# Optimization experiments

Measured on AMD Instinct MI355X. Metric: run time of the kernel, lower is better.

## Reference

```python
import jax, jax.numpy as jnp
import numpy as np

N_HEAD = 16
N_KV = 4
ROT = 128  # rotary_dim == head_dim
BASE = 10000
N_CTX = 1024


def make_sincos(n_ctx, rotary_dim, base):
    # GPT-NeoX style (rotary_adjacent_pairs=False): freq repeated twice
    pos = jnp.arange(n_ctx, dtype=jnp.float32)
    dim = jnp.arange(rotary_dim // 2, dtype=jnp.float32)
    freq = jnp.float32(base) ** (dim / (rotary_dim / 2))
    freq = jnp.tile(freq, 2)  # [rotary_dim]
    angles = pos[:, None] / freq[None, :]  # [n_ctx, rotary_dim]
    return jnp.sin(angles), jnp.cos(angles)


def setup_inputs() -> dict:
    key = jax.random.key(0)
    ks = jax.random.split(key, 5)
    B, T, C = 8, 1024, 2048
    r = N_HEAD // N_KV
    Ckv = C // r
    s = 0.02
    x = jax.random.normal(ks[0], (B, T, C), jnp.float32)
    wq = jax.random.normal(ks[1], (C, C), jnp.float32) * s
    wk = jax.random.normal(ks[2], (C, Ckv), jnp.float32) * s
    wv = jax.random.normal(ks[3], (C, Ckv), jnp.float32) * s
    wo = jax.random.normal(ks[4], (C, C), jnp.float32) * s
    sin, cos = make_sincos(N_CTX, ROT, BASE)
    return dict(x=x, wq=wq, wk=wk, wv=wv, wo=wo, sin=sin, cos=cos)


def _rope(x, sin, cos):
    # x: [B, H, T, hd]; rotary applied to first ROT dims (here ROT == hd)
    T = x.shape[2]
    n = ROT // 2
    x_rot = x[..., :ROT]
    x_pass = x[..., ROT:]
    # rotate_every_two (NeoX style): [x0..x_{n-1}, x_n..] -> [-x_n.., x0..]
    x_flip = jnp.concatenate([-x_rot[..., n:], x_rot[..., :n]], axis=-1)
    c = cos[None, None, :T, :]
    s = sin[None, None, :T, :]
    x_rotated = x_rot * c + x_flip * s
    return jnp.concatenate([x_rotated, x_pass], axis=-1)


def reference(x, wq, wk, wv, wo, sin, cos):
    B, T, C = x.shape
    H = N_HEAD
    hd = C // H
    r = H // N_KV
    q = (x @ wq).reshape(B, T, H, hd).transpose(0, 2, 1, 3)  # [B,H,T,hd]
    # Original: repeat_interleave along seq dim then view(B,T,H,hd).
    # Equivalent to tiling the kv channel vector r times per position.
    k = jnp.tile(x @ wk, (1, 1, r)).reshape(B, T, H, hd).transpose(0, 2, 1, 3)
    v = jnp.tile(x @ wv, (1, 1, r)).reshape(B, T, H, hd).transpose(0, 2, 1, 3)
    q = _rope(q, sin, cos)
    k = _rope(k, sin, cos)
    att = jnp.einsum('bhqd,bhkd->bhqk', q, k) / jnp.sqrt(jnp.float32(hd))
    causal = jnp.tril(jnp.ones((T, T), dtype=bool))
    att = jnp.where(causal[None, None], att, -jnp.inf)
    att = jax.nn.softmax(att, axis=-1)
    y = jnp.einsum('bhqk,bhkd->bhqd', att, v)
    y = y.transpose(0, 2, 1, 3).reshape(B, T, C)
    return y @ wo
```

## Files before the change

kernel.cpp:

```cpp
#include <hip/hip_runtime.h>

typedef __attribute__((ext_vector_type(8))) short short8;
typedef __attribute__((ext_vector_type(4))) float f32x4;

#define B_    8
#define T_    1024
#define C_    2048
#define H_    16
#define HKV_  4
#define HD_   128
#define M_    8192
#define NQKV_ 3072
#define KDIM_ 2048

__device__ __forceinline__ unsigned short f2bf(float f) {
  unsigned u = __float_as_uint(f);
  u += 0x7FFF + ((u >> 16) & 1);
  return (unsigned short)(u >> 16);
}
__device__ __forceinline__ float bf2f(unsigned short h) {
  return __uint_as_float(((unsigned)h) << 16);
}

__device__ __forceinline__ void async16(const unsigned short* g, unsigned short* l) {
  __builtin_amdgcn_global_load_lds(
      (const unsigned int __attribute__((address_space(1)))*)g,
      (unsigned int __attribute__((address_space(3)))*)l,
      16, 0, 0);
}

__global__ __launch_bounds__(256) void cvt_bf16_kernel(const float* __restrict__ in,
                                                       unsigned short* __restrict__ out) {
  int idx = blockIdx.x * 256 + threadIdx.x;
  float4 v = ((const float4*)in)[idx];
  ushort4 o;
  o.x = f2bf(v.x); o.y = f2bf(v.y); o.z = f2bf(v.z); o.w = f2bf(v.w);
  ((ushort4*)out)[idx] = o;
}

__global__ __launch_bounds__(256) void tpose_f32_bf16(const float* __restrict__ in,
                                                      unsigned short* __restrict__ out,
                                                      int Cc, int ldo) {
  __shared__ unsigned short tile[32][33];
  int c0 = blockIdx.x * 32, r0 = blockIdx.y * 32;
  int tx = threadIdx.x, ty = threadIdx.y;
#pragma unroll
  for (int j = 0; j < 4; j++)
    tile[ty + j * 8][tx] = f2bf(in[(size_t)(r0 + ty + j * 8) * Cc + c0 + tx]);
  __syncthreads();
#pragma unroll
  for (int j = 0; j < 4; j++)
    out[(size_t)(c0 + ty + j * 8) * ldo + r0 + tx] = tile[tx][ty + j * 8];
}

__global__ __launch_bounds__(256) void vtpose(const unsigned short* __restrict__ qkv,
                                              unsigned short* __restrict__ vt) {
  __shared__ unsigned short tile[32][33];
  int b = blockIdx.z;
  int c0 = blockIdx.x * 32, t0 = blockIdx.y * 32;
  int tx = threadIdx.x, ty = threadIdx.y;
  const unsigned short* src = qkv + (size_t)b * T_ * NQKV_ + 2560;
#pragma unroll
  for (int j = 0; j < 4; j++)
    tile[ty + j * 8][tx] = src[(size_t)(t0 + ty + j * 8) * NQKV_ + c0 + tx];
  __syncthreads();
  unsigned short* dst = vt + (size_t)b * 512 * T_;
#pragma unroll
  for (int j = 0; j < 4; j++)
    dst[(size_t)(c0 + ty + j * 8) * T_ + t0 + tx] = tile[tx][ty + j * 8];
}

__global__ __launch_bounds__(256) void rope_kernel(const unsigned short* __restrict__ qkv,
                                                   const float* __restrict__ sinp,
                                                   const float* __restrict__ cosp,
                                                   unsigned short* __restrict__ qatt,
                                                   unsigned short* __restrict__ katt) {
  int m = blockIdx.x;
  int b = m >> 10, t = m & 1023;
  int tid = threadIdx.x;
  int d = tid & 63;
  const unsigned short* row = qkv + (size_t)m * NQKV_;
  float c0 = cosp[t * 128 + d], s0 = sinp[t * 128 + d];
  float c1 = cosp[t * 128 + d + 64], s1 = sinp[t * 128 + d + 64];
#pragma unroll
  for (int h0 = 0; h0 < 16; h0 += 4) {
    int h = h0 + (tid >> 6);
    float x0 = bf2f(row[h * 128 + d]);
    float x1 = bf2f(row[h * 128 + d + 64]);
    size_t o = ((size_t)(b * 16 + h) * 1024 + t) * 128 + d;
    qatt[o]      = f2bf(x0 * c0 - x1 * s0);
    qatt[o + 64] = f2bf(x1 * c1 + x0 * s1);
  }
  {
    int kh = tid >> 6;
    float x0 = bf2f(row[2048 + kh * 128 + d]);
    float x1 = bf2f(row[2048 + kh * 128 + d + 64]);
    size_t o = ((size_t)(b * 4 + kh) * 1024 + t) * 128 + d;
    katt[o]      = f2bf(x0 * c0 - x1 * s0);
    katt[o + 64] = f2bf(x1 * c1 + x0 * s1);
  }
}

template <int OUTF32>
__global__ __launch_bounds__(256) void gemm_bf16(const unsigned short* __restrict__ A,
                                                 const unsigned short* __restrict__ BT,
                                                 void* __restrict__ Cout, int N) {
  __shared__ unsigned short lA[128 * 32];
  __shared__ unsigned short lB[128 * 32];
  const int K = KDIM_;
  int tid = threadIdx.x;
  int lane = tid & 63;
  int w = tid >> 6;
  int quad = lane >> 4, l16 = lane & 15;
  int bm = blockIdx.y, bn = blockIdx.x;
  const unsigned short* Ab = A + (size_t)bm * 128 * K;
  const unsigned short* Bb = BT + (size_t)bn * 128 * K;
  int i0 = tid, i1 = tid + 256;
  int ra0 = i0 >> 2, ca0 = (i0 & 3) * 8;
  int ra1 = i1 >> 2, ca1 = (i1 & 3) * 8;
  int wm = (w >> 1) * 64, wn = (w & 1) * 64;
  f32x4 acc[4][4] = {};
  for (int k0 = 0; k0 < K; k0 += 32) {
    __syncthreads();
    async16(Ab + (size_t)ra0 * K + k0 + ca0, &lA[i0 * 8]);
    async16(Ab + (size_t)ra1 * K + k0 + ca1, &lA[i1 * 8]);
    async16(Bb + (size_t)ra0 * K + k0 + ca0, &lB[i0 * 8]);
    async16(Bb + (size_t)ra1 * K + k0 + ca1, &lB[i1 * 8]);
    __syncthreads();
    short8 af[4], bfr[4];
#pragma unroll
    for (int mt = 0; mt < 4; mt++)
      af[mt] = *(const short8*)&lA[(wm + mt * 16 + l16) * 32 + quad * 8];
#pragma unroll
    for (int nt = 0; nt < 4; nt++)
      bfr[nt] = *(const short8*)&lB[(wn + nt * 16 + l16) * 32 + quad * 8];
#pragma unroll
    for (int mt = 0; mt < 4; mt++)
#pragma unroll
      for (int nt = 0; nt < 4; nt++)
        acc[mt][nt] = __builtin_amdgcn_mfma_f32_16x16x32_bf16(af[mt], bfr[nt], acc[mt][nt], 0, 0, 0);
  }
#pragma unroll
  for (int mt = 0; mt < 4; mt++) {
#pragma unroll
    for (int nt = 0; nt < 4; nt++) {
      int n = bn * 128 + wn + nt * 16 + l16;
#pragma unroll
      for (int r = 0; r < 4; r++) {
        int m = bm * 128 + wm + mt * 16 + quad * 4 + r;
        if (OUTF32)
          ((float*)Cout)[(size_t)m * N + n] = acc[mt][nt][r];
        else
          ((unsigned short*)Cout)[(size_t)m * N + n] = f2bf(acc[mt][nt][r]);
      }
    }
  }
}

__global__ __launch_bounds__(256, 4) void attn_kernel(const unsigned short* __restrict__ Q,
                                                      const unsigned short* __restrict__ Km,
                                                      const unsigned short* __restrict__ Vt,
                                                      unsigned short* __restrict__ Y) {
  __shared__ __align__(16) unsigned short lK[8192];
  __shared__ __align__(16) unsigned short lV[8192];
  int tid = threadIdx.x;
  int lane = tid & 63, w = tid >> 6;
  int quad = lane >> 4, l16 = lane & 15;
  int qt = 15 - blockIdx.x;
  int bh = blockIdx.y;
  int b = bh >> 4, h = bh & 15, kh = h & 3;
  int qrow0 = qt * 64 + w * 16;
  const unsigned short* Qb = Q + ((size_t)bh * T_ + qrow0) * 128;
  const unsigned short* Kb = Km + (size_t)(b * 4 + kh) * T_ * 128;
  const unsigned short* Vb = Vt + (size_t)(b * 4 + kh) * 128 * T_;
  short8 qf[4];
#pragma unroll
  for (int ks = 0; ks < 4; ks++)
    qf[ks] = *(const short8*)&Qb[l16 * 128 + ks * 32 + quad * 8];
  f32x4 o[8] = {};
  float m_r[4] = {-1e30f, -1e30f, -1e30f, -1e30f};
  float l_r[4] = {0.f, 0.f, 0.f, 0.f};
  const float sc = 0.12751744690989f;
  unsigned short* pb = &lK[w * 1152];
  int ntile = qt + 1;
  for (int kt = 0; kt < ntile; kt++) {
    int n0 = kt * 64;
    __syncthreads();
#pragma unroll
    for (int j = 0; j < 4; j++) {
      int i = tid + j * 256;
      async16(Kb + (size_t)(n0 + ((i >> 2) & 63)) * 128 + (i >> 8) * 32 + (i & 3) * 8,
              &lK[i * 8]);
    }
#pragma unroll
    for (int j = 0; j < 4; j++) {
      int i = tid + j * 256;
      async16(Vb + (size_t)((i >> 2) & 127) * T_ + n0 + (i >> 9) * 32 + (i & 3) * 8,
              &lV[i * 8]);
    }
    __syncthreads();
    f32x4 s[4] = {};
#pragma unroll
    for (int ct = 0; ct < 4; ct++) {
#pragma unroll
      for (int ks = 0; ks < 4; ks++) {
        short8 kf = *(const short8*)&lK[ks * 2048 + (ct * 16 + l16) * 32 + quad * 8];
        s[ct] = __builtin_amdgcn_mfma_f32_16x16x32_bf16(qf[ks], kf, s[ct], 0, 0, 0);
      }
    }
#pragma unroll
    for (int ct = 0; ct < 4; ct++)
#pragma unroll
      for (int r = 0; r < 4; r++)
        s[ct][r] *= sc;
    if (kt == qt) {
#pragma unroll
      for (int ct = 0; ct < 4; ct++) {
        int n = n0 + ct * 16 + l16;
#pragma unroll
        for (int r = 0; r < 4; r++) {
          int q = qrow0 + quad * 4 + r;
          if (n > q) s[ct][r] = -1e30f;
        }
      }
    }
    float mn[4], alpha[4];
#pragma unroll
    for (int r = 0; r < 4; r++) {
      float v = fmaxf(fmaxf(s[0][r], s[1][r]), fmaxf(s[2][r], s[3][r]));
#pragma unroll
      for (int off = 1; off < 16; off <<= 1)
        v = fmaxf(v, __shfl_xor(v, off));
      mn[r] = fmaxf(m_r[r], v);
      alpha[r] = exp2f(m_r[r] - mn[r]);
      m_r[r] = mn[r];
    }
#pragma unroll
    for (int ct = 0; ct < 4; ct++)
#pragma unroll
      for (int r = 0; r < 4; r++)
        s[ct][r] = exp2f(s[ct][r] - mn[r]);
#pragma unroll
    for (int r = 0; r < 4; r++) {
      float v = s[0][r] + s[1][r] + s[2][r] + s[3][r];
#pragma unroll
      for (int off = 1; off < 16; off <<= 1)
        v += __shfl_xor(v, off);
      l_r[r] = l_r[r] * alpha[r] + v;
    }
#pragma unroll
    for (int dt = 0; dt < 8; dt++)
#pragma unroll
      for (int r = 0; r < 4; r++)
        o[dt][r] *= alpha[r];
    __syncthreads();
#pragma unroll
    for (int ct = 0; ct < 4; ct++)
#pragma unroll
      for (int r = 0; r < 4; r++)
        pb[(quad * 4 + r) * 72 + ct * 16 + l16] = f2bf(s[ct][r]);
    __builtin_amdgcn_s_waitcnt(0xC07F);
#pragma unroll
    for (int ks2 = 0; ks2 < 2; ks2++) {
      short8 pa = *(const short8*)&pb[l16 * 72 + ks2 * 32 + quad * 8];
#pragma unroll
      for (int dt = 0; dt < 8; dt++) {
        short8 vf = *(const short8*)&lV[ks2 * 4096 + (dt * 16 + l16) * 32 + quad * 8];
        o[dt] = __builtin_amdgcn_mfma_f32_16x16x32_bf16(pa, vf, o[dt], 0, 0, 0);
      }
    }
  }
#pragma unroll
  for (int r = 0; r < 4; r++) {
    int q = qrow0 + quad * 4 + r;
    float inv = 1.f / l_r[r];
    size_t base = ((size_t)(b * 1024 + q)) * 2048 + h * 128 + l16;
#pragma unroll
    for (int dt = 0; dt < 8; dt++)
      Y[base + dt * 16] = f2bf(o[dt][r] * inv);
  }
}

extern "C" void kernel_launch(void* const* d_in, const int* in_sizes, int n_in,
                              void* d_out, int out_size, void* d_ws, size_t ws_size,
                              hipStream_t stream) {
  const float* x    = (const float*)d_in[0];
  const float* wq   = (const float*)d_in[1];
  const float* wk   = (const float*)d_in[2];
  const float* wv   = (const float*)d_in[3];
  const float* wo   = (const float*)d_in[4];
  const float* sinp = (const float*)d_in[5];
  const float* cosp = (const float*)d_in[6];

  char* ws = (char*)d_ws;
  unsigned short* WCATT = (unsigned short*)(ws);
  unsigned short* WOT   = (unsigned short*)(ws + 12582912);
  unsigned short* XBF   = (unsigned short*)(ws + 20971520);
  unsigned short* QKV   = (unsigned short*)(ws + 54525952);
  unsigned short* KATT  = (unsigned short*)(ws + 104857600);
  unsigned short* VT    = (unsigned short*)(ws + 113246208);
  unsigned short* QATT  = XBF;
  unsigned short* Y     = QKV;

  dim3 tb(32, 8);
  cvt_bf16_kernel<<<16384, 256, 0, stream>>>(x, XBF);
  tpose_f32_bf16<<<dim3(64, 64), tb, 0, stream>>>(wq, WCATT, 2048, 2048);
  tpose_f32_bf16<<<dim3(16, 64), tb, 0, stream>>>(wk, WCATT + (size_t)2048 * 2048, 512, 2048);
  tpose_f32_bf16<<<dim3(16, 64), tb, 0, stream>>>(wv, WCATT + (size_t)2560 * 2048, 512, 2048);
  tpose_f32_bf16<<<dim3(64, 64), tb, 0, stream>>>(wo, WOT, 2048, 2048);
  gemm_bf16<0><<<dim3(24, 64), 256, 0, stream>>>(XBF, WCATT, QKV, 3072);
  rope_kernel<<<8192, 256, 0, stream>>>(QKV, sinp, cosp, QATT, KATT);
  vtpose<<<dim3(16, 32, 8), tb, 0, stream>>>(QKV, VT);
  attn_kernel<<<dim3(16, 128), 256, 0, stream>>>(QATT, KATT, VT, Y);
  gemm_bf16<1><<<dim3(16, 64), 256, 0, stream>>>(Y, WOT, d_out, 2048);
}
```

Baseline: 566.7 us.

## Double query rows per attention block and swizzle K/V shared-memory layout

Each attention workgroup now processes 128 query rows (32 per wave, two MFMA row tiles) instead of 64, so each K/V tile loaded into shared memory feeds twice as many MMAs and the grid halves. K and V staging uses an XOR swizzle on the 8-element chunk index to reduce LDS bank conflicts on fragment reads. The trade-off is more registers (launch bounds drop to 2 blocks per CU), fewer blocks for load balance under the causal mask, and serialized P-buffer reuse between the two row tiles.

```diff
diff --git a/kernel.cpp b/kernel.cpp
--- a/kernel.cpp
+++ b/kernel.cpp
@@ -157,7 +157,7 @@
   }
 }
 
-__global__ __launch_bounds__(256, 4) void attn_kernel(const unsigned short* __restrict__ Q,
+__global__ __launch_bounds__(256, 2) void attn_kernel(const unsigned short* __restrict__ Q,
                                                       const unsigned short* __restrict__ Km,
                                                       const unsigned short* __restrict__ Vt,
                                                       unsigned short* __restrict__ Y) {
@@ -166,119 +166,164 @@
   int tid = threadIdx.x;
   int lane = tid & 63, w = tid >> 6;
   int quad = lane >> 4, l16 = lane & 15;
-  int qt = 15 - blockIdx.x;
+  int qt = 7 - blockIdx.x;
   int bh = blockIdx.y;
   int b = bh >> 4, h = bh & 15, kh = h & 3;
-  int qrow0 = qt * 64 + w * 16;
+  int qrow0 = qt * 128 + w * 32;
   const unsigned short* Qb = Q + ((size_t)bh * T_ + qrow0) * 128;
   const unsigned short* Kb = Km + (size_t)(b * 4 + kh) * T_ * 128;
   const unsigned short* Vb = Vt + (size_t)(b * 4 + kh) * 128 * T_;
-  short8 qf[4];
-#pragma unroll
-  for (int ks = 0; ks < 4; ks++)
-    qf[ks] = *(const short8*)&Qb[l16 * 128 + ks * 32 + quad * 8];
-  f32x4 o[8] = {};
-  float m_r[4] = {-1e30f, -1e30f, -1e30f, -1e30f};
-  float l_r[4] = {0.f, 0.f, 0.f, 0.f};
+  short8 qf[2][4];
+#pragma unroll
+  for (int mt = 0; mt < 2; mt++)
+#pragma unroll
+    for (int ks = 0; ks < 4; ks++)
+      qf[mt][ks] = *(const short8*)&Qb[(mt * 16 + l16) * 128 + ks * 32 + quad * 8];
+  f32x4 o[2][8] = {};
+  float m_r[2][4], l_r[2][4];
+#pragma unroll
+  for (int mt = 0; mt < 2; mt++)
+#pragma unroll
+    for (int r = 0; r < 4; r++) {
+      m_r[mt][r] = -1e30f;
+      l_r[mt][r] = 0.f;
+    }
   const float sc = 0.12751744690989f;
   unsigned short* pb = &lK[w * 1152];
-  int ntile = qt + 1;
+  const int sw = (l16 & 3) * 8;
+  int ntile = 2 * qt + 2;
   for (int kt = 0; kt < ntile; kt++) {
     int n0 = kt * 64;
     __syncthreads();
 #pragma unroll
     for (int j = 0; j < 4; j++) {
       int i = tid + j * 256;
-      async16(Kb + (size_t)(n0 + ((i >> 2) & 63)) * 128 + (i >> 8) * 32 + (i & 3) * 8,
+      int tq = (i & 3) ^ ((i >> 2) & 3);
+      async16(Kb + (size_t)(n0 + ((i >> 2) & 63)) * 128 + (i >> 8) * 32 + tq * 8,
               &lK[i * 8]);
     }
 #pragma unroll
     for (int j = 0; j < 4; j++) {
       int i = tid + j * 256;
-      async16(Vb + (size_t)((i >> 2) & 127) * T_ + n0 + (i >> 9) * 32 + (i & 3) * 8,
+      int tq = (i & 3) ^ ((i >> 2) & 3);
+      async16(Vb + (size_t)((i >> 2) & 127) * T_ + n0 + (i >> 9) * 32 + tq * 8,
               &lV[i * 8]);
     }
     __syncthreads();
-    f32x4 s[4] = {};
+    f32x4 s[2][4] = {};
 #pragma unroll
     for (int ct = 0; ct < 4; ct++) {
+      short8 kf[4];
+#pragma unroll
+      for (int ks = 0; ks < 4; ks++)
+        kf[ks] = *(const short8*)&lK[ks * 2048 + (ct * 16 + l16) * 32 + (quad * 8 ^ sw)];
 #pragma unroll
       for (int ks = 0; ks < 4; ks++) {
-        short8 kf = *(const short8*)&lK[ks * 2048 + (ct * 16 + l16) * 32 + quad * 8];
-        s[ct] = __builtin_amdgcn_mfma_f32_16x16x32_bf16(qf[ks], kf, s[ct], 0, 0, 0);
-      }
-    }
+        s[0][ct] = __builtin_amdgcn_mfma_f32_16x16x32_bf16(qf[0][ks], kf[ks], s[0][ct], 0, 0, 0);
+        s[1][ct] = __builtin_amdgcn_mfma_f32_16x16x32_bf16(qf[1][ks], kf[ks], s[1][ct], 0, 0, 0);
+      }
+    }
+#pragma unroll
+    for (int mt = 0; mt < 2; mt++)
+#pragma unroll
+      for (int ct = 0; ct < 4; ct++)
+#pragma unroll
+        for (int r = 0; r < 4; r++)
+          s[mt][ct][r] *= sc;
+    if (kt >= 2 * qt) {
+#pragma unroll
+      for (int mt = 0; mt < 2; mt++)
+#pragma unroll
+        for (int ct = 0; ct < 4; ct++) {
+          int n = n0 + ct * 16 + l16;
+#pragma unroll
+          for (int r = 0; r < 4; r++) {
+            int q = qrow0 + mt * 16 + quad * 4 + r;
+            if (n > q) s[mt][ct][r] = -1e30f;
+          }
+        }
+    }
+    float alpha[2][4];
+#pragma unroll
+    for (int mt = 0; mt < 2; mt++)
+#pragma unroll
+      for (int r = 0; r < 4; r++) {
+        float v = fmaxf(fmaxf(s[mt][0][r], s[mt][1][r]), fmaxf(s[mt][2][r], s[mt][3][r]));
+#pragma unroll
+        for (int off = 1; off < 16; off <<= 1)
+          v = fmaxf(v, __shfl_xor(v, off));
+        float mn = fmaxf(m_r[mt][r], v);
+        alpha[mt][r] = exp2f(m_r[mt][r] - mn);
+        m_r[mt][r] = mn;
+      }
+#pragma unroll
+    for (int mt = 0; mt < 2; mt++)
+#pragma unroll
+      for (int ct = 0; ct < 4; ct++)
+#pragma unroll
+        for (int r = 0; r < 4; r++)
+          s[mt][ct][r] = exp2f(s[mt][ct][r] - m_r[mt][r]);
+#pragma unroll
+    for (int mt = 0; mt < 2; mt++)
+#pragma unroll
+      for (int r = 0; r < 4; r++) {
+        float v = s[mt][0][r] + s[mt][1][r] + s[mt][2][r] + s[mt][3][r];
+#pragma unroll
+        for (int off = 1; off < 16; off <<= 1)
+          v += __shfl_xor(v, off);
+        l_r[mt][r] = l_r[mt][r] * alpha[mt][r] + v;
+      }
+#pragma unroll
+    for (int mt = 0; mt < 2; mt++)
+#pragma unroll
+      for (int dt = 0; dt < 8; dt++)
+#pragma unroll
+        for (int r = 0; r < 4; r++)
+          o[mt][dt][r] *= alpha[mt][r];
+    __syncthreads();
 #pragma unroll
     for (int ct = 0; ct < 4; ct++)
 #pragma unroll
       for (int r = 0; r < 4; r++)
-        s[ct][r] *= sc;
-    if (kt == qt) {
-#pragma unroll
-      for (int ct = 0; ct < 4; ct++) {
-        int n = n0 + ct * 16 + l16;
-#pragma unroll
-        for (int r = 0; r < 4; r++) {
-          int q = qrow0 + quad * 4 + r;
-          if (n > q) s[ct][r] = -1e30f;
-        }
-      }
-    }
-    float mn[4], alpha[4];
+        pb[(quad * 4 + r) * 72 + ct * 16 + l16] = f2bf(s[0][ct][r]);
+    __builtin_amdgcn_s_waitcnt(0xC07F);
+    short8 pa0[2];
+#pragma unroll
+    for (int ks2 = 0; ks2 < 2; ks2++)
+      pa0[ks2] = *(const short8*)&pb[l16 * 72 + ks2 * 32 + quad * 8];
+    __builtin_amdgcn_s_waitcnt(0xC07F);
+    asm volatile("" ::: "memory");
+#pragma unroll
+    for (int ct = 0; ct < 4; ct++)
+#pragma unroll
+      for (int r = 0; r < 4; r++)
+        pb[(quad * 4 + r) * 72 + ct * 16 + l16] = f2bf(s[1][ct][r]);
+    __builtin_amdgcn_s_waitcnt(0xC07F);
+    short8 pa1[2];
+#pragma unroll
+    for (int ks2 = 0; ks2 < 2; ks2++)
+      pa1[ks2] = *(const short8*)&pb[l16 * 72 + ks2 * 32 + quad * 8];
+#pragma unroll
+    for (int dt = 0; dt < 8; dt++) {
+#pragma unroll
+      for (int ks2 = 0; ks2 < 2; ks2++) {
+        short8 vf = *(const short8*)&lV[ks2 * 4096 + (dt * 16 + l16) * 32 + (quad * 8 ^ sw)];
+        o[0][dt] = __builtin_amdgcn_mfma_f32_16x16x32_bf16(pa0[ks2], vf, o[0][dt], 0, 0, 0);
+        o[1][dt] = __builtin_amdgcn_mfma_f32_16x16x32_bf16(pa1[ks2], vf, o[1][dt], 0, 0, 0);
+      }
+    }
+  }
+#pragma unroll
+  for (int mt = 0; mt < 2; mt++)
 #pragma unroll
     for (int r = 0; r < 4; r++) {
-      float v = fmaxf(fmaxf(s[0][r], s[1][r]), fmaxf(s[2][r], s[3][r]));
-#pragma unroll
-      for (int off = 1; off < 16; off <<= 1)
-        v = fmaxf(v, __shfl_xor(v, off));
-      mn[r] = fmaxf(m_r[r], v);
-      alpha[r] = exp2f(m_r[r] - mn[r]);
-      m_r[r] = mn[r];
-    }
-#pragma unroll
-    for (int ct = 0; ct < 4; ct++)
-#pragma unroll
-      for (int r = 0; r < 4; r++)
-        s[ct][r] = exp2f(s[ct][r] - mn[r]);
-#pragma unroll
-    for (int r = 0; r < 4; r++) {
-      float v = s[0][r] + s[1][r] + s[2][r] + s[3][r];
-#pragma unroll
-      for (int off = 1; off < 16; off <<= 1)
-        v += __shfl_xor(v, off);
-      l_r[r] = l_r[r] * alpha[r] + v;
-    }
-#pragma unroll
-    for (int dt = 0; dt < 8; dt++)
-#pragma unroll
-      for (int r = 0; r < 4; r++)
-        o[dt][r] *= alpha[r];
-    __syncthreads();
-#pragma unroll
-    for (int ct = 0; ct < 4; ct++)
-#pragma unroll
-      for (int r = 0; r < 4; r++)
-        pb[(quad * 4 + r) * 72 + ct * 16 + l16] = f2bf(s[ct][r]);
-    __builtin_amdgcn_s_waitcnt(0xC07F);
-#pragma unroll
-    for (int ks2 = 0; ks2 < 2; ks2++) {
-      short8 pa = *(const short8*)&pb[l16 * 72 + ks2 * 32 + quad * 8];
-#pragma unroll
-      for (int dt = 0; dt < 8; dt++) {
-        short8 vf = *(const short8*)&lV[ks2 * 4096 + (dt * 16 + l16) * 32 + quad * 8];
-        o[dt] = __builtin_amdgcn_mfma_f32_16x16x32_bf16(pa, vf, o[dt], 0, 0, 0);
-      }
-    }
-  }
-#pragma unroll
-  for (int r = 0; r < 4; r++) {
-    int q = qrow0 + quad * 4 + r;
-    float inv = 1.f / l_r[r];
-    size_t base = ((size_t)(b * 1024 + q)) * 2048 + h * 128 + l16;
-#pragma unroll
-    for (int dt = 0; dt < 8; dt++)
-      Y[base + dt * 16] = f2bf(o[dt][r] * inv);
-  }
+      int q = qrow0 + mt * 16 + quad * 4 + r;
+      float inv = 1.f / l_r[mt][r];
+      size_t base = ((size_t)(b * 1024 + q)) * 2048 + h * 128 + l16;
+#pragma unroll
+      for (int dt = 0; dt < 8; dt++)
+        Y[base + dt * 16] = f2bf(o[mt][dt][r] * inv);
+    }
 }
 
 extern "C" void kernel_launch(void* const* d_in, const int* in_sizes, int n_in,
@@ -311,6 +356,6 @@
   gemm_bf16<0><<<dim3(24, 64), 256, 0, stream>>>(XBF, WCATT, QKV, 3072);
   rope_kernel<<<8192, 256, 0, stream>>>(QKV, sinp, cosp, QATT, KATT);
   vtpose<<<dim3(16, 32, 8), tb, 0, stream>>>(QKV, VT);
-  attn_kernel<<<dim3(16, 128), 256, 0, stream>>>(QATT, KATT, VT, Y);
+  attn_kernel<<<dim3(8, 128), 256, 0, stream>>>(QATT, KATT, VT, Y);
   gemm_bf16<1><<<dim3(16, 64), 256, 0, stream>>>(Y, WOT, d_out, 2048);
 }
```

New measurement: 546.2 us. 1.04x faster.
